# Performance work log

Measured on AMD Instinct MI355X. Metric: run time of the kernel, lower is better.

## Reference

```python
import jax, jax.numpy as jnp
import numpy as np

N = 100000  # num nodes
E = 1600000  # num edges
D_IN = 64
D_OUT = 64


def setup_inputs() -> dict:
    key = jax.random.key(0)
    k = jax.random.split(key, 8)
    x = jax.random.normal(k[0], (N, D_IN), dtype=jnp.float32)
    edge_index = jax.random.randint(k[1], (2, E), 0, N, dtype=jnp.int64)
    s1 = 1.0 / np.sqrt(D_IN)
    s2 = 1.0 / np.sqrt(D_OUT)
    W1 = jax.random.uniform(k[2], (D_IN, D_OUT), jnp.float32, -s1, s1)
    b1 = jax.random.uniform(k[3], (D_OUT,), jnp.float32, -s1, s1)
    W2 = jax.random.uniform(k[4], (D_OUT, D_OUT), jnp.float32, -s2, s2)
    b2 = jax.random.uniform(k[5], (D_OUT,), jnp.float32, -s2, s2)
    eps = jnp.asarray(0.0, dtype=jnp.float32)  # learnable (train_eps=True)
    return {"x": x, "edge_index": edge_index, "W1": W1, "b1": b1, "W2": W2, "b2": b2, "eps": eps}


def reference(x, edge_index, W1, b1, W2, b2, eps):
    src, dst = edge_index[0], edge_index[1]
    # sum-aggregate neighbor features: agg[i] = sum_{(j->i)} x[j]
    agg = jax.ops.segment_sum(x[src], dst, num_segments=N)  # [N, D_IN]
    h = (1.0 + eps) * x + agg
    h = jax.nn.relu(h @ W1 + b1)
    return h @ W2 + b2
```

## Files before the change

### kernel.cpp

```cpp
#include <hip/hip_runtime.h>

#define NN 100000
#define NE 1600000
#define D  64
#define NBK 512
#define NPB 196
#define RPL 8
#define CAPR 512
#define CHUNK 2048
#define NCH ((NE + CHUNK - 1) / CHUNK)
#define CVTB ((NN * D / 4 + 255) / 256)


typedef unsigned short u16;
typedef __attribute__((ext_vector_type(8))) short bf16x8;
typedef __attribute__((ext_vector_type(4))) float f32x4;

__device__ __forceinline__ u16 f32_to_bf16_rn(float f) {
    unsigned u = __float_as_uint(f);
    return (u16)((u + 0x7FFF + ((u >> 16) & 1)) >> 16);
}
__device__ __forceinline__ float bflo(unsigned w) {
    return __uint_as_float(w << 16);
}
__device__ __forceinline__ float bfhi(unsigned w) {
    return __uint_as_float(w & 0xFFFF0000u);
}

__global__ __launch_bounds__(256) void bin_cvt_kernel(const float* __restrict__ x,
                                                      u16* __restrict__ xb,
                                                      const int* __restrict__ ei,
                                                      int* __restrict__ cursor,
                                                      int* __restrict__ bins) {
    __shared__ int lc[NBK];
    __shared__ int lbase[NBK];
    const int t = threadIdx.x;

    if (blockIdx.x >= NCH) {
        int i = ((blockIdx.x - NCH) * 256 + t) * 4;
        if (i < NN * D) {
            float4 v = *(const float4*)(x + i);
            ushort4 o;
            o.x = f32_to_bf16_rn(v.x);
            o.y = f32_to_bf16_rn(v.y);
            o.z = f32_to_bf16_rn(v.z);
            o.w = f32_to_bf16_rn(v.w);
            *(ushort4*)(xb + i) = o;
        }
        return;
    }

    const int base = blockIdx.x * CHUNK;
    const int rep  = blockIdx.x & (RPL - 1);

    for (int i = t; i < NBK; i += 256) lc[i] = 0;
    __syncthreads();
    #pragma unroll 4
    for (int j = 0; j < CHUNK / 256; ++j) {
        int e = base + t + j * 256;
        if (e < NE) atomicAdd(&lc[(unsigned)ei[NE + e] / NPB], 1);
    }
    __syncthreads();
    for (int i = t; i < NBK; i += 256) {
        int c = lc[i];
        lbase[i] = c ? atomicAdd(&cursor[rep * NBK + i], c) : 0;
        lc[i] = 0;
    }
    __syncthreads();
    #pragma unroll 4
    for (int j = 0; j < CHUNK / 256; ++j) {
        int e = base + t + j * 256;
        if (e < NE) {
            int src = ei[e];
            int dst = ei[NE + e];
            int b   = (unsigned)dst / NPB;
            int loc = dst - b * NPB;
            int o   = atomicAdd(&lc[b], 1);
            int pos = lbase[b] + o;
            if (pos < CAPR)
                bins[(b * RPL + rep) * CAPR + pos] = (loc << 17) | src;
        }
    }
}

__global__ __launch_bounds__(1024) void agg_kernel(const float* __restrict__ x,
                                                   const u16* __restrict__ xb,
                                                   const float* __restrict__ eps,
                                                   const int* __restrict__ cursor,
                                                   const int* __restrict__ bins,
                                                   float* __restrict__ out) {
    __shared__ int sorted[RPL * CAPR];
    __shared__ int tmp[256];
    __shared__ int off[256];
    __shared__ int cur[256];
    const int b    = blockIdx.x;
    const int t    = threadIdx.x;
    const int lane = t & 63;
    const int w    = t >> 6;
    const float e1 = 1.0f + *eps;

    if (t < 256) tmp[t] = 0;
    __syncthreads();
    int nrep[RPL];
    #pragma unroll
    for (int r = 0; r < RPL; ++r) nrep[r] = min(cursor[r * NBK + b], CAPR);
    #pragma unroll
    for (int r = 0; r < RPL; ++r) {
        const int rb = (b * RPL + r) * CAPR;
        for (int i = t; i < nrep[r]; i += 1024)
            atomicAdd(&tmp[bins[rb + i] >> 17], 1);
    }
    __syncthreads();
    int v = (t < 256) ? tmp[t] : 0;
    for (int o = 1; o < 256; o <<= 1) {
        int u = (t < 256 && t >= o) ? tmp[t - o] : 0;
        __syncthreads();
        if (t < 256) tmp[t] += u;
        __syncthreads();
    }
    if (t < 256) { off[t] = tmp[t] - v; cur[t] = tmp[t] - v; }
    __syncthreads();
    #pragma unroll
    for (int r = 0; r < RPL; ++r) {
        const int rb = (b * RPL + r) * CAPR;
        for (int i = t; i < nrep[r]; i += 1024) {
            int pk  = bins[rb + i];
            int pos = atomicAdd(&cur[pk >> 17], 1);
            sorted[pos] = pk & 0x1FFFF;
        }
    }
    __syncthreads();

    const int g = lane >> 4;
    const int c = lane & 15;
    #pragma unroll
    for (int j = 0; j < 13; ++j) {
        int r = w + 16 * j;
        if (r < NPB) {
            int node = b * NPB + r;
            if (node < NN) {
                float4 a;
                if (g == 0) {
                    float4 xv = *(const float4*)(x + node * D + 4 * c);
                    a.x = e1 * xv.x; a.y = e1 * xv.y;
                    a.z = e1 * xv.z; a.w = e1 * xv.w;
                } else {
                    a.x = a.y = a.z = a.w = 0.f;
                }
                int p  = off[r];
                int pe = off[r + 1];
                for (; p + 8 <= pe; p += 8) {
                    int e0 = sorted[p + g];
                    int e1i = sorted[p + 4 + g];
                    uint2 v0 = *(const uint2*)(xb + e0 * D + 4 * c);
                    uint2 v1 = *(const uint2*)(xb + e1i * D + 4 * c);
                    a.x += bflo(v0.x) + bflo(v1.x);
                    a.y += bfhi(v0.x) + bfhi(v1.x);
                    a.z += bflo(v0.y) + bflo(v1.y);
                    a.w += bfhi(v0.y) + bfhi(v1.y);
                }
                for (; p + 4 <= pe; p += 4) {
                    int e0 = sorted[p + g];
                    uint2 v0 = *(const uint2*)(xb + e0 * D + 4 * c);
                    a.x += bflo(v0.x);
                    a.y += bfhi(v0.x);
                    a.z += bflo(v0.y);
                    a.w += bfhi(v0.y);
                }
                if (p < pe) {
                    bool ok = (p + g) < pe;
                    int e0 = sorted[ok ? p + g : p];
                    uint2 v0 = *(const uint2*)(xb + e0 * D + 4 * c);
                    a.x += ok ? bflo(v0.x) : 0.f;
                    a.y += ok ? bfhi(v0.x) : 0.f;
                    a.z += ok ? bflo(v0.y) : 0.f;
                    a.w += ok ? bfhi(v0.y) : 0.f;
                }
                a.x += __shfl_xor(a.x, 16); a.x += __shfl_xor(a.x, 32);
                a.y += __shfl_xor(a.y, 16); a.y += __shfl_xor(a.y, 32);
                a.z += __shfl_xor(a.z, 16); a.z += __shfl_xor(a.z, 32);
                a.w += __shfl_xor(a.w, 16); a.w += __shfl_xor(a.w, 32);
                if (g == 0)
                    *(float4*)(out + node * D + 4 * c) = a;
            }
        }
    }
}

#define WSTR 72
__global__ __launch_bounds__(256, 2) void mlp_mfma_kernel(
        float* __restrict__ h,
        const float* __restrict__ W1, const float* __restrict__ b1,
        const float* __restrict__ W2, const float* __restrict__ b2) {
    __shared__ u16 wt1[D * WSTR];
    __shared__ u16 wt2[D * WSTR];
    __shared__ u16 lds[4][16 * WSTR];
    const int lane = threadIdx.x & 63;
    const int wv   = threadIdx.x >> 6;
    const int m    = lane & 15;
    const int q    = lane >> 4;
    u16* tile = &lds[wv][0];

    for (int i = threadIdx.x; i < D * D; i += 256) {
        int k = i >> 6, n = i & 63;
        wt1[n * WSTR + k] = f32_to_bf16_rn(W1[i]);
        wt2[n * WSTR + k] = f32_to_bf16_rn(W2[i]);
    }
    __syncthreads();

    bf16x8 wb1[4][2], wb2[4][2];
    #pragma unroll
    for (int t = 0; t < 4; ++t)
        #pragma unroll
        for (int s = 0; s < 2; ++s) {
            const int o = (t * 16 + m) * WSTR + s * 32 + q * 8;
            wb1[t][s] = *(const bf16x8*)&wt1[o];
            wb2[t][s] = *(const bf16x8*)&wt2[o];
        }
    float bias1[4], bias2[4];
    #pragma unroll
    for (int t = 0; t < 4; ++t) {
        bias1[t] = b1[t * 16 + m];
        bias2[t] = b2[t * 16 + m];
    }

    const int wave = blockIdx.x * 4 + wv;
    const int nw   = gridDim.x * 4;
    for (int ti = wave; ti < NN / 16; ti += nw) {
        const int rowbase = ti * 16;

        bf16x8 a1f[2];
        #pragma unroll
        for (int s = 0; s < 2; ++s) {
            const float* p = h + (rowbase + m) * D + s * 32 + q * 8;
            float4 v0 = *(const float4*)p;
            float4 v1 = *(const float4*)(p + 4);
            bf16x8 f;
            f[0] = (short)f32_to_bf16_rn(v0.x);
            f[1] = (short)f32_to_bf16_rn(v0.y);
            f[2] = (short)f32_to_bf16_rn(v0.z);
            f[3] = (short)f32_to_bf16_rn(v0.w);
            f[4] = (short)f32_to_bf16_rn(v1.x);
            f[5] = (short)f32_to_bf16_rn(v1.y);
            f[6] = (short)f32_to_bf16_rn(v1.z);
            f[7] = (short)f32_to_bf16_rn(v1.w);
            a1f[s] = f;
        }

        #pragma unroll
        for (int t = 0; t < 4; ++t) {
            f32x4 cc = {0.f, 0.f, 0.f, 0.f};
            cc = __builtin_amdgcn_mfma_f32_16x16x32_bf16(a1f[0], wb1[t][0], cc, 0, 0, 0);
            cc = __builtin_amdgcn_mfma_f32_16x16x32_bf16(a1f[1], wb1[t][1], cc, 0, 0, 0);
            #pragma unroll
            for (int r = 0; r < 4; ++r) {
                float vv = fmaxf(cc[r] + bias1[t], 0.0f);
                tile[(q * 4 + r) * WSTR + t * 16 + m] = f32_to_bf16_rn(vv);
            }
        }

        bf16x8 a2f[2];
        #pragma unroll
        for (int s = 0; s < 2; ++s)
            a2f[s] = *(const bf16x8*)&tile[m * WSTR + s * 32 + q * 8];

        #pragma unroll
        for (int t = 0; t < 4; ++t) {
            f32x4 cc = {0.f, 0.f, 0.f, 0.f};
            cc = __builtin_amdgcn_mfma_f32_16x16x32_bf16(a2f[0], wb2[t][0], cc, 0, 0, 0);
            cc = __builtin_amdgcn_mfma_f32_16x16x32_bf16(a2f[1], wb2[t][1], cc, 0, 0, 0);
            #pragma unroll
            for (int r = 0; r < 4; ++r)
                h[(rowbase + q * 4 + r) * D + t * 16 + m] = cc[r] + bias2[t];
        }
    }
}

extern "C" void kernel_launch(void* const* d_in, const int* in_sizes, int n_in,
                              void* d_out, int out_size, void* d_ws, size_t ws_size,
                              hipStream_t stream) {
    const float* x   = (const float*)d_in[0];
    const int*   ei  = (const int*)d_in[1];
    const float* W1  = (const float*)d_in[2];
    const float* b1  = (const float*)d_in[3];
    const float* W2  = (const float*)d_in[4];
    const float* b2  = (const float*)d_in[5];
    const float* eps = (const float*)d_in[6];
    float*       out = (float*)d_out;

    int* cursor = (int*)d_ws;
    int* bins   = cursor + RPL * NBK;
    u16* xb     = (u16*)(bins + NBK * RPL * CAPR);

    hipMemsetAsync(cursor, 0, RPL * NBK * sizeof(int), stream);
    bin_cvt_kernel<<<NCH + CVTB, 256, 0, stream>>>(x, xb, ei, cursor, bins);
    agg_kernel<<<NBK, 1024, 0, stream>>>(x, xb, eps, cursor, bins, out);
    mlp_mfma_kernel<<<1024, 256, 0, stream>>>(out, W1, b1, W2, b2);
}
```

Measured before the change: 159.0 us.

## Fuse aggregation and MLP into one kernel using per-block LDS tile

Merges the aggregation and the two-layer MFMA MLP into a single kernel. Each block aggregates its 192 nodes into a bf16 LDS tile, then 12 waves run both matmuls on 16-row slices and write the final output directly. This removes the fp32 intermediate round trip through global memory and one kernel launch. In exchange, every block reloads and converts the weights, LDS use per block grows, and the bucket geometry is retuned (NPB 192, NBK 521). The bf16 conversion of x is also widened to 16 elements per thread.

```diff
diff --git a/kernel.cpp b/kernel.cpp
--- a/kernel.cpp
+++ b/kernel.cpp
@@ -3,13 +3,14 @@
 #define NN 100000
 #define NE 1600000
 #define D  64
-#define NBK 512
-#define NPB 196
+#define NPB 192
+#define NBK 521
 #define RPL 8
 #define CAPR 512
 #define CHUNK 2048
 #define NCH ((NE + CHUNK - 1) / CHUNK)
-#define CVTB ((NN * D / 4 + 255) / 256)
+#define CVTB ((NN * D / 16 + 255) / 256)
+#define WSTR 72
 
 
 typedef unsigned short u16;
@@ -19,6 +20,9 @@
 __device__ __forceinline__ u16 f32_to_bf16_rn(float f) {
     unsigned u = __float_as_uint(f);
     return (u16)((u + 0x7FFF + ((u >> 16) & 1)) >> 16);
+}
+__device__ __forceinline__ unsigned pk2(float lo, float hi) {
+    return (unsigned)f32_to_bf16_rn(lo) | ((unsigned)f32_to_bf16_rn(hi) << 16);
 }
 __device__ __forceinline__ float bflo(unsigned w) {
     return __uint_as_float(w << 16);
@@ -37,15 +41,19 @@
     const int t = threadIdx.x;
 
     if (blockIdx.x >= NCH) {
-        int i = ((blockIdx.x - NCH) * 256 + t) * 4;
+        int i = ((blockIdx.x - NCH) * 256 + t) * 16;
         if (i < NN * D) {
-            float4 v = *(const float4*)(x + i);
-            ushort4 o;
-            o.x = f32_to_bf16_rn(v.x);
-            o.y = f32_to_bf16_rn(v.y);
-            o.z = f32_to_bf16_rn(v.z);
-            o.w = f32_to_bf16_rn(v.w);
-            *(ushort4*)(xb + i) = o;
+            float4 a = *(const float4*)(x + i);
+            float4 b = *(const float4*)(x + i + 4);
+            float4 c = *(const float4*)(x + i + 8);
+            float4 d = *(const float4*)(x + i + 12);
+            uint4 o1, o2;
+            o1.x = pk2(a.x, a.y); o1.y = pk2(a.z, a.w);
+            o1.z = pk2(b.x, b.y); o1.w = pk2(b.z, b.w);
+            o2.x = pk2(c.x, c.y); o2.y = pk2(c.z, c.w);
+            o2.z = pk2(d.x, d.y); o2.w = pk2(d.z, d.w);
+            *(uint4*)(xb + i) = o1;
+            *(uint4*)(xb + i + 8) = o2;
         }
         return;
     }
@@ -83,21 +91,33 @@
     }
 }
 
-__global__ __launch_bounds__(1024) void agg_kernel(const float* __restrict__ x,
-                                                   const u16* __restrict__ xb,
-                                                   const float* __restrict__ eps,
-                                                   const int* __restrict__ cursor,
-                                                   const int* __restrict__ bins,
-                                                   float* __restrict__ out) {
+__global__ __launch_bounds__(1024, 8) void agg_mlp_kernel(
+        const float* __restrict__ x,
+        const u16* __restrict__ xb,
+        const float* __restrict__ eps,
+        const int* __restrict__ cursor,
+        const int* __restrict__ bins,
+        const float* __restrict__ W1, const float* __restrict__ b1,
+        const float* __restrict__ W2, const float* __restrict__ b2,
+        float* __restrict__ out) {
     __shared__ int sorted[RPL * CAPR];
     __shared__ int tmp[256];
     __shared__ int off[256];
     __shared__ int cur[256];
+    __shared__ u16 wt1[D * WSTR];
+    __shared__ u16 wt2[D * WSTR];
+    __shared__ u16 htile[NPB * WSTR];
     const int b    = blockIdx.x;
     const int t    = threadIdx.x;
     const int lane = t & 63;
     const int w    = t >> 6;
     const float e1 = 1.0f + *eps;
+
+    for (int i = t; i < D * D; i += 1024) {
+        int k = i >> 6, n = i & 63;
+        wt1[n * WSTR + k] = f32_to_bf16_rn(W1[i]);
+        wt2[n * WSTR + k] = f32_to_bf16_rn(W2[i]);
+    }
 
     if (t < 256) tmp[t] = 0;
     __syncthreads();
@@ -134,144 +154,113 @@
     const int g = lane >> 4;
     const int c = lane & 15;
     #pragma unroll
-    for (int j = 0; j < 13; ++j) {
+    for (int j = 0; j < 12; ++j) {
         int r = w + 16 * j;
-        if (r < NPB) {
-            int node = b * NPB + r;
-            if (node < NN) {
-                float4 a;
-                if (g == 0) {
-                    float4 xv = *(const float4*)(x + node * D + 4 * c);
-                    a.x = e1 * xv.x; a.y = e1 * xv.y;
-                    a.z = e1 * xv.z; a.w = e1 * xv.w;
-                } else {
-                    a.x = a.y = a.z = a.w = 0.f;
-                }
-                int p  = off[r];
-                int pe = off[r + 1];
-                for (; p + 8 <= pe; p += 8) {
-                    int e0 = sorted[p + g];
-                    int e1i = sorted[p + 4 + g];
-                    uint2 v0 = *(const uint2*)(xb + e0 * D + 4 * c);
-                    uint2 v1 = *(const uint2*)(xb + e1i * D + 4 * c);
-                    a.x += bflo(v0.x) + bflo(v1.x);
-                    a.y += bfhi(v0.x) + bfhi(v1.x);
-                    a.z += bflo(v0.y) + bflo(v1.y);
-                    a.w += bfhi(v0.y) + bfhi(v1.y);
-                }
-                for (; p + 4 <= pe; p += 4) {
-                    int e0 = sorted[p + g];
-                    uint2 v0 = *(const uint2*)(xb + e0 * D + 4 * c);
-                    a.x += bflo(v0.x);
-                    a.y += bfhi(v0.x);
-                    a.z += bflo(v0.y);
-                    a.w += bfhi(v0.y);
-                }
-                if (p < pe) {
-                    bool ok = (p + g) < pe;
-                    int e0 = sorted[ok ? p + g : p];
-                    uint2 v0 = *(const uint2*)(xb + e0 * D + 4 * c);
-                    a.x += ok ? bflo(v0.x) : 0.f;
-                    a.y += ok ? bfhi(v0.x) : 0.f;
-                    a.z += ok ? bflo(v0.y) : 0.f;
-                    a.w += ok ? bfhi(v0.y) : 0.f;
-                }
-                a.x += __shfl_xor(a.x, 16); a.x += __shfl_xor(a.x, 32);
-                a.y += __shfl_xor(a.y, 16); a.y += __shfl_xor(a.y, 32);
-                a.z += __shfl_xor(a.z, 16); a.z += __shfl_xor(a.z, 32);
-                a.w += __shfl_xor(a.w, 16); a.w += __shfl_xor(a.w, 32);
-                if (g == 0)
-                    *(float4*)(out + node * D + 4 * c) = a;
-            }
-        }
-    }
-}
-
-#define WSTR 72
-__global__ __launch_bounds__(256, 2) void mlp_mfma_kernel(
-        float* __restrict__ h,
-        const float* __restrict__ W1, const float* __restrict__ b1,
-        const float* __restrict__ W2, const float* __restrict__ b2) {
-    __shared__ u16 wt1[D * WSTR];
-    __shared__ u16 wt2[D * WSTR];
-    __shared__ u16 lds[4][16 * WSTR];
-    const int lane = threadIdx.x & 63;
-    const int wv   = threadIdx.x >> 6;
-    const int m    = lane & 15;
-    const int q    = lane >> 4;
-    u16* tile = &lds[wv][0];
-
-    for (int i = threadIdx.x; i < D * D; i += 256) {
-        int k = i >> 6, n = i & 63;
-        wt1[n * WSTR + k] = f32_to_bf16_rn(W1[i]);
-        wt2[n * WSTR + k] = f32_to_bf16_rn(W2[i]);
-    }
-    __syncthreads();
-
-    bf16x8 wb1[4][2], wb2[4][2];
-    #pragma unroll
-    for (int t = 0; t < 4; ++t)
-        #pragma unroll
-        for (int s = 0; s < 2; ++s) {
-            const int o = (t * 16 + m) * WSTR + s * 32 + q * 8;
-            wb1[t][s] = *(const bf16x8*)&wt1[o];
-            wb2[t][s] = *(const bf16x8*)&wt2[o];
-        }
-    float bias1[4], bias2[4];
-    #pragma unroll
-    for (int t = 0; t < 4; ++t) {
-        bias1[t] = b1[t * 16 + m];
-        bias2[t] = b2[t * 16 + m];
-    }
-
-    const int wave = blockIdx.x * 4 + wv;
-    const int nw   = gridDim.x * 4;
-    for (int ti = wave; ti < NN / 16; ti += nw) {
-        const int rowbase = ti * 16;
+        int node = b * NPB + r;
+        if (node < NN) {
+            float4 a;
+            if (g == 0) {
+                float4 xv = *(const float4*)(x + node * D + 4 * c);
+                a.x = e1 * xv.x; a.y = e1 * xv.y;
+                a.z = e1 * xv.z; a.w = e1 * xv.w;
+            } else {
+                a.x = a.y = a.z = a.w = 0.f;
+            }
+            int p  = off[r];
+            int pe = off[r + 1];
+            for (; p + 8 <= pe; p += 8) {
+                int e0 = sorted[p + g];
+                int e1i = sorted[p + 4 + g];
+                uint2 v0 = *(const uint2*)(xb + e0 * D + 4 * c);
+                uint2 v1 = *(const uint2*)(xb + e1i * D + 4 * c);
+                a.x += bflo(v0.x) + bflo(v1.x);
+                a.y += bfhi(v0.x) + bfhi(v1.x);
+                a.z += bflo(v0.y) + bflo(v1.y);
+                a.w += bfhi(v0.y) + bfhi(v1.y);
+            }
+            for (; p + 4 <= pe; p += 4) {
+                int e0 = sorted[p + g];
+                uint2 v0 = *(const uint2*)(xb + e0 * D + 4 * c);
+                a.x += bflo(v0.x);
+                a.y += bfhi(v0.x);
+                a.z += bflo(v0.y);
+                a.w += bfhi(v0.y);
+            }
+            if (p < pe) {
+                bool ok = (p + g) < pe;
+                int e0 = sorted[ok ? p + g : p];
+                uint2 v0 = *(const uint2*)(xb + e0 * D + 4 * c);
+                a.x += ok ? bflo(v0.x) : 0.f;
+                a.y += ok ? bfhi(v0.x) : 0.f;
+                a.z += ok ? bflo(v0.y) : 0.f;
+                a.w += ok ? bfhi(v0.y) : 0.f;
+            }
+            a.x += __shfl_xor(a.x, 16); a.x += __shfl_xor(a.x, 32);
+            a.y += __shfl_xor(a.y, 16); a.y += __shfl_xor(a.y, 32);
+            a.z += __shfl_xor(a.z, 16); a.z += __shfl_xor(a.z, 32);
+            a.w += __shfl_xor(a.w, 16); a.w += __shfl_xor(a.w, 32);
+            if (g == 0) {
+                ushort4 o;
+                o.x = f32_to_bf16_rn(a.x);
+                o.y = f32_to_bf16_rn(a.y);
+                o.z = f32_to_bf16_rn(a.z);
+                o.w = f32_to_bf16_rn(a.w);
+                *(ushort4*)&htile[r * WSTR + 4 * c] = o;
+            }
+        }
+    }
+    __syncthreads();
+
+    if (w < 12) {
+        const int m  = lane & 15;
+        const int q  = lane >> 4;
+        const int rowbase = b * NPB + w * 16;
+        float bias1[4], bias2[4];
+        #pragma unroll
+        for (int tt = 0; tt < 4; ++tt) {
+            bias1[tt] = b1[tt * 16 + m];
+            bias2[tt] = b2[tt * 16 + m];
+        }
 
         bf16x8 a1f[2];
         #pragma unroll
-        for (int s = 0; s < 2; ++s) {
-            const float* p = h + (rowbase + m) * D + s * 32 + q * 8;
-            float4 v0 = *(const float4*)p;
-            float4 v1 = *(const float4*)(p + 4);
-            bf16x8 f;
-            f[0] = (short)f32_to_bf16_rn(v0.x);
-            f[1] = (short)f32_to_bf16_rn(v0.y);
-            f[2] = (short)f32_to_bf16_rn(v0.z);
-            f[3] = (short)f32_to_bf16_rn(v0.w);
-            f[4] = (short)f32_to_bf16_rn(v1.x);
-            f[5] = (short)f32_to_bf16_rn(v1.y);
-            f[6] = (short)f32_to_bf16_rn(v1.z);
-            f[7] = (short)f32_to_bf16_rn(v1.w);
-            a1f[s] = f;
-        }
-
-        #pragma unroll
-        for (int t = 0; t < 4; ++t) {
+        for (int s = 0; s < 2; ++s)
+            a1f[s] = *(const bf16x8*)&htile[(w * 16 + m) * WSTR + s * 32 + q * 8];
+
+        #pragma unroll
+        for (int tt = 0; tt < 4; ++tt) {
+            const int o = (tt * 16 + m) * WSTR + q * 8;
+            bf16x8 w0 = *(const bf16x8*)&wt1[o];
+            bf16x8 w1v = *(const bf16x8*)&wt1[o + 32];
             f32x4 cc = {0.f, 0.f, 0.f, 0.f};
-            cc = __builtin_amdgcn_mfma_f32_16x16x32_bf16(a1f[0], wb1[t][0], cc, 0, 0, 0);
-            cc = __builtin_amdgcn_mfma_f32_16x16x32_bf16(a1f[1], wb1[t][1], cc, 0, 0, 0);
+            cc = __builtin_amdgcn_mfma_f32_16x16x32_bf16(a1f[0], w0, cc, 0, 0, 0);
+            cc = __builtin_amdgcn_mfma_f32_16x16x32_bf16(a1f[1], w1v, cc, 0, 0, 0);
             #pragma unroll
             for (int r = 0; r < 4; ++r) {
-                float vv = fmaxf(cc[r] + bias1[t], 0.0f);
-                tile[(q * 4 + r) * WSTR + t * 16 + m] = f32_to_bf16_rn(vv);
+                float vv = fmaxf(cc[r] + bias1[tt], 0.0f);
+                htile[(w * 16 + q * 4 + r) * WSTR + tt * 16 + m] = f32_to_bf16_rn(vv);
             }
         }
 
         bf16x8 a2f[2];
         #pragma unroll
         for (int s = 0; s < 2; ++s)
-            a2f[s] = *(const bf16x8*)&tile[m * WSTR + s * 32 + q * 8];
-
-        #pragma unroll
-        for (int t = 0; t < 4; ++t) {
+            a2f[s] = *(const bf16x8*)&htile[(w * 16 + m) * WSTR + s * 32 + q * 8];
+
+        #pragma unroll
+        for (int tt = 0; tt < 4; ++tt) {
+            const int o = (tt * 16 + m) * WSTR + q * 8;
+            bf16x8 w0 = *(const bf16x8*)&wt2[o];
+            bf16x8 w1v = *(const bf16x8*)&wt2[o + 32];
             f32x4 cc = {0.f, 0.f, 0.f, 0.f};
-            cc = __builtin_amdgcn_mfma_f32_16x16x32_bf16(a2f[0], wb2[t][0], cc, 0, 0, 0);
-            cc = __builtin_amdgcn_mfma_f32_16x16x32_bf16(a2f[1], wb2[t][1], cc, 0, 0, 0);
+            cc = __builtin_amdgcn_mfma_f32_16x16x32_bf16(a2f[0], w0, cc, 0, 0, 0);
+            cc = __builtin_amdgcn_mfma_f32_16x16x32_bf16(a2f[1], w1v, cc, 0, 0, 0);
             #pragma unroll
-            for (int r = 0; r < 4; ++r)
-                h[(rowbase + q * 4 + r) * D + t * 16 + m] = cc[r] + bias2[t];
+            for (int r = 0; r < 4; ++r) {
+                int grow = rowbase + q * 4 + r;
+                if (grow < NN)
+                    out[grow * D + tt * 16 + m] = cc[r] + bias2[tt];
+            }
         }
     }
 }
@@ -294,6 +283,6 @@
 
     hipMemsetAsync(cursor, 0, RPL * NBK * sizeof(int), stream);
     bin_cvt_kernel<<<NCH + CVTB, 256, 0, stream>>>(x, xb, ei, cursor, bins);
-    agg_kernel<<<NBK, 1024, 0, stream>>>(x, xb, eps, cursor, bins, out);
-    mlp_mfma_kernel<<<1024, 256, 0, stream>>>(out, W1, b1, W2, b2);
-}
+    agg_mlp_kernel<<<NBK, 1024, 0, stream>>>(x, xb, eps, cursor, bins,
+                                             W1, b1, W2, b2, out);
+}
```

New measurement: 185.9 us. 16.9% more time.

## Store aggregated features as bf16, widen conversion, cache dst indices, retune bucketing

Applied to the files above, without the earlier changes.

The aggregation kernel now writes its result as bf16 into a workspace buffer, and the MLP kernel reads that buffer directly instead of reading fp32 and converting. This halves the intermediate traffic between the two kernels. The x-to-bf16 conversion processes 16 elements per thread with wide packed stores. The binning kernel loads destination indices once into registers. Buckets shrink to 192 nodes (521 buckets) and the MLP grid is halved. The extra rounding of the pre-MLP activations was already done inside the MLP before, so accuracy is essentially unchanged.

```diff
diff --git a/kernel.cpp b/kernel.cpp
--- a/kernel.cpp
+++ b/kernel.cpp
@@ -3,13 +3,15 @@
 #define NN 100000
 #define NE 1600000
 #define D  64
-#define NBK 512
-#define NPB 196
+#define NPB 192
+#define NBK 521
 #define RPL 8
 #define CAPR 512
 #define CHUNK 2048
+#define EPT (CHUNK / 256)
 #define NCH ((NE + CHUNK - 1) / CHUNK)
-#define CVTB ((NN * D / 4 + 255) / 256)
+#define CVTB ((NN * D / 16 + 255) / 256)
+#define WSTR 72
 
 
 typedef unsigned short u16;
@@ -19,6 +21,9 @@
 __device__ __forceinline__ u16 f32_to_bf16_rn(float f) {
     unsigned u = __float_as_uint(f);
     return (u16)((u + 0x7FFF + ((u >> 16) & 1)) >> 16);
+}
+__device__ __forceinline__ unsigned pk2(float lo, float hi) {
+    return (unsigned)f32_to_bf16_rn(lo) | ((unsigned)f32_to_bf16_rn(hi) << 16);
 }
 __device__ __forceinline__ float bflo(unsigned w) {
     return __uint_as_float(w << 16);
@@ -37,15 +42,19 @@
     const int t = threadIdx.x;
 
     if (blockIdx.x >= NCH) {
-        int i = ((blockIdx.x - NCH) * 256 + t) * 4;
+        int i = ((blockIdx.x - NCH) * 256 + t) * 16;
         if (i < NN * D) {
-            float4 v = *(const float4*)(x + i);
-            ushort4 o;
-            o.x = f32_to_bf16_rn(v.x);
-            o.y = f32_to_bf16_rn(v.y);
-            o.z = f32_to_bf16_rn(v.z);
-            o.w = f32_to_bf16_rn(v.w);
-            *(ushort4*)(xb + i) = o;
+            float4 a = *(const float4*)(x + i);
+            float4 b = *(const float4*)(x + i + 4);
+            float4 c = *(const float4*)(x + i + 8);
+            float4 d = *(const float4*)(x + i + 12);
+            uint4 o1, o2;
+            o1.x = pk2(a.x, a.y); o1.y = pk2(a.z, a.w);
+            o1.z = pk2(b.x, b.y); o1.w = pk2(b.z, b.w);
+            o2.x = pk2(c.x, c.y); o2.y = pk2(c.z, c.w);
+            o2.z = pk2(d.x, d.y); o2.w = pk2(d.z, d.w);
+            *(uint4*)(xb + i) = o1;
+            *(uint4*)(xb + i + 8) = o2;
         }
         return;
     }
@@ -53,13 +62,18 @@
     const int base = blockIdx.x * CHUNK;
     const int rep  = blockIdx.x & (RPL - 1);
 
+    int dsts[EPT];
+    #pragma unroll
+    for (int j = 0; j < EPT; ++j) {
+        int e = base + t + j * 256;
+        dsts[j] = (e < NE) ? ei[NE + e] : -1;
+    }
+
     for (int i = t; i < NBK; i += 256) lc[i] = 0;
     __syncthreads();
-    #pragma unroll 4
-    for (int j = 0; j < CHUNK / 256; ++j) {
-        int e = base + t + j * 256;
-        if (e < NE) atomicAdd(&lc[(unsigned)ei[NE + e] / NPB], 1);
-    }
+    #pragma unroll
+    for (int j = 0; j < EPT; ++j)
+        if (dsts[j] >= 0) atomicAdd(&lc[(unsigned)dsts[j] / NPB], 1);
     __syncthreads();
     for (int i = t; i < NBK; i += 256) {
         int c = lc[i];
@@ -67,12 +81,11 @@
         lc[i] = 0;
     }
     __syncthreads();
-    #pragma unroll 4
-    for (int j = 0; j < CHUNK / 256; ++j) {
-        int e = base + t + j * 256;
-        if (e < NE) {
-            int src = ei[e];
-            int dst = ei[NE + e];
+    #pragma unroll
+    for (int j = 0; j < EPT; ++j) {
+        if (dsts[j] >= 0) {
+            int src = ei[base + t + j * 256];
+            int dst = dsts[j];
             int b   = (unsigned)dst / NPB;
             int loc = dst - b * NPB;
             int o   = atomicAdd(&lc[b], 1);
@@ -88,7 +101,7 @@
                                                    const float* __restrict__ eps,
                                                    const int* __restrict__ cursor,
                                                    const int* __restrict__ bins,
-                                                   float* __restrict__ out) {
+                                                   u16* __restrict__ hb) {
     __shared__ int sorted[RPL * CAPR];
     __shared__ int tmp[256];
     __shared__ int off[256];
@@ -134,62 +147,65 @@
     const int g = lane >> 4;
     const int c = lane & 15;
     #pragma unroll
-    for (int j = 0; j < 13; ++j) {
+    for (int j = 0; j < 12; ++j) {
         int r = w + 16 * j;
-        if (r < NPB) {
-            int node = b * NPB + r;
-            if (node < NN) {
-                float4 a;
-                if (g == 0) {
-                    float4 xv = *(const float4*)(x + node * D + 4 * c);
-                    a.x = e1 * xv.x; a.y = e1 * xv.y;
-                    a.z = e1 * xv.z; a.w = e1 * xv.w;
-                } else {
-                    a.x = a.y = a.z = a.w = 0.f;
-                }
-                int p  = off[r];
-                int pe = off[r + 1];
-                for (; p + 8 <= pe; p += 8) {
-                    int e0 = sorted[p + g];
-                    int e1i = sorted[p + 4 + g];
-                    uint2 v0 = *(const uint2*)(xb + e0 * D + 4 * c);
-                    uint2 v1 = *(const uint2*)(xb + e1i * D + 4 * c);
-                    a.x += bflo(v0.x) + bflo(v1.x);
-                    a.y += bfhi(v0.x) + bfhi(v1.x);
-                    a.z += bflo(v0.y) + bflo(v1.y);
-                    a.w += bfhi(v0.y) + bfhi(v1.y);
-                }
-                for (; p + 4 <= pe; p += 4) {
-                    int e0 = sorted[p + g];
-                    uint2 v0 = *(const uint2*)(xb + e0 * D + 4 * c);
-                    a.x += bflo(v0.x);
-                    a.y += bfhi(v0.x);
-                    a.z += bflo(v0.y);
-                    a.w += bfhi(v0.y);
-                }
-                if (p < pe) {
-                    bool ok = (p + g) < pe;
-                    int e0 = sorted[ok ? p + g : p];
-                    uint2 v0 = *(const uint2*)(xb + e0 * D + 4 * c);
-                    a.x += ok ? bflo(v0.x) : 0.f;
-                    a.y += ok ? bfhi(v0.x) : 0.f;
-                    a.z += ok ? bflo(v0.y) : 0.f;
-                    a.w += ok ? bfhi(v0.y) : 0.f;
-                }
-                a.x += __shfl_xor(a.x, 16); a.x += __shfl_xor(a.x, 32);
-                a.y += __shfl_xor(a.y, 16); a.y += __shfl_xor(a.y, 32);
-                a.z += __shfl_xor(a.z, 16); a.z += __shfl_xor(a.z, 32);
-                a.w += __shfl_xor(a.w, 16); a.w += __shfl_xor(a.w, 32);
-                if (g == 0)
-                    *(float4*)(out + node * D + 4 * c) = a;
-            }
-        }
-    }
-}
-
-#define WSTR 72
+        int node = b * NPB + r;
+        if (node < NN) {
+            float4 a;
+            if (g == 0) {
+                float4 xv = *(const float4*)(x + node * D + 4 * c);
+                a.x = e1 * xv.x; a.y = e1 * xv.y;
+                a.z = e1 * xv.z; a.w = e1 * xv.w;
+            } else {
+                a.x = a.y = a.z = a.w = 0.f;
+            }
+            int p  = off[r];
+            int pe = off[r + 1];
+            for (; p + 8 <= pe; p += 8) {
+                int e0 = sorted[p + g];
+                int e1i = sorted[p + 4 + g];
+                uint2 v0 = *(const uint2*)(xb + e0 * D + 4 * c);
+                uint2 v1 = *(const uint2*)(xb + e1i * D + 4 * c);
+                a.x += bflo(v0.x) + bflo(v1.x);
+                a.y += bfhi(v0.x) + bfhi(v1.x);
+                a.z += bflo(v0.y) + bflo(v1.y);
+                a.w += bfhi(v0.y) + bfhi(v1.y);
+            }
+            for (; p + 4 <= pe; p += 4) {
+                int e0 = sorted[p + g];
+                uint2 v0 = *(const uint2*)(xb + e0 * D + 4 * c);
+                a.x += bflo(v0.x);
+                a.y += bfhi(v0.x);
+                a.z += bflo(v0.y);
+                a.w += bfhi(v0.y);
+            }
+            if (p < pe) {
+                bool ok = (p + g) < pe;
+                int e0 = sorted[ok ? p + g : p];
+                uint2 v0 = *(const uint2*)(xb + e0 * D + 4 * c);
+                a.x += ok ? bflo(v0.x) : 0.f;
+                a.y += ok ? bfhi(v0.x) : 0.f;
+                a.z += ok ? bflo(v0.y) : 0.f;
+                a.w += ok ? bfhi(v0.y) : 0.f;
+            }
+            a.x += __shfl_xor(a.x, 16); a.x += __shfl_xor(a.x, 32);
+            a.y += __shfl_xor(a.y, 16); a.y += __shfl_xor(a.y, 32);
+            a.z += __shfl_xor(a.z, 16); a.z += __shfl_xor(a.z, 32);
+            a.w += __shfl_xor(a.w, 16); a.w += __shfl_xor(a.w, 32);
+            if (g == 0) {
+                ushort4 o;
+                o.x = f32_to_bf16_rn(a.x);
+                o.y = f32_to_bf16_rn(a.y);
+                o.z = f32_to_bf16_rn(a.z);
+                o.w = f32_to_bf16_rn(a.w);
+                *(ushort4*)(hb + node * D + 4 * c) = o;
+            }
+        }
+    }
+}
+
 __global__ __launch_bounds__(256, 2) void mlp_mfma_kernel(
-        float* __restrict__ h,
+        const u16* __restrict__ hb, float* __restrict__ out,
         const float* __restrict__ W1, const float* __restrict__ b1,
         const float* __restrict__ W2, const float* __restrict__ b2) {
     __shared__ u16 wt1[D * WSTR];
@@ -231,21 +247,8 @@
 
         bf16x8 a1f[2];
         #pragma unroll
-        for (int s = 0; s < 2; ++s) {
-            const float* p = h + (rowbase + m) * D + s * 32 + q * 8;
-            float4 v0 = *(const float4*)p;
-            float4 v1 = *(const float4*)(p + 4);
-            bf16x8 f;
-            f[0] = (short)f32_to_bf16_rn(v0.x);
-            f[1] = (short)f32_to_bf16_rn(v0.y);
-            f[2] = (short)f32_to_bf16_rn(v0.z);
-            f[3] = (short)f32_to_bf16_rn(v0.w);
-            f[4] = (short)f32_to_bf16_rn(v1.x);
-            f[5] = (short)f32_to_bf16_rn(v1.y);
-            f[6] = (short)f32_to_bf16_rn(v1.z);
-            f[7] = (short)f32_to_bf16_rn(v1.w);
-            a1f[s] = f;
-        }
+        for (int s = 0; s < 2; ++s)
+            a1f[s] = *(const bf16x8*)(hb + (rowbase + m) * D + s * 32 + q * 8);
 
         #pragma unroll
         for (int t = 0; t < 4; ++t) {
@@ -271,7 +274,7 @@
             cc = __builtin_amdgcn_mfma_f32_16x16x32_bf16(a2f[1], wb2[t][1], cc, 0, 0, 0);
             #pragma unroll
             for (int r = 0; r < 4; ++r)
-                h[(rowbase + q * 4 + r) * D + t * 16 + m] = cc[r] + bias2[t];
+                out[(rowbase + q * 4 + r) * D + t * 16 + m] = cc[r] + bias2[t];
         }
     }
 }
@@ -291,9 +294,10 @@
     int* cursor = (int*)d_ws;
     int* bins   = cursor + RPL * NBK;
     u16* xb     = (u16*)(bins + NBK * RPL * CAPR);
+    u16* hb     = xb + NN * D;
 
     hipMemsetAsync(cursor, 0, RPL * NBK * sizeof(int), stream);
     bin_cvt_kernel<<<NCH + CVTB, 256, 0, stream>>>(x, xb, ei, cursor, bins);
-    agg_kernel<<<NBK, 1024, 0, stream>>>(x, xb, eps, cursor, bins, out);
-    mlp_mfma_kernel<<<1024, 256, 0, stream>>>(out, W1, b1, W2, b2);
-}
+    agg_kernel<<<NBK, 1024, 0, stream>>>(x, xb, eps, cursor, bins, hb);
+    mlp_mfma_kernel<<<512, 256, 0, stream>>>(hb, out, W1, b1, W2, b2);
+}
```

New measurement: 191.2 us. +20.2%, slower.
